# Kernel optimization log

Hardware: AMD Instinct MI355X
Metric: run time of the kernel (lower is better)

Reference implementation:

```python
import jax, jax.numpy as jnp
import numpy as np
from jax import lax

# Static problem dims (match input_specs)
B, N, F, H, C = 128, 512, 512, 256, 10
EPG = 8192            # edges per graph
K1, K2 = 256, 128      # pooling_ratio=0.5 applied twice
LAMB = 1.0
BN_EPS = 1e-5


def setup_inputs() -> dict:
    key = jax.random.key(0)
    ks = jax.random.split(key, 24)
    x = jax.random.normal(ks[0], (B * N, F), dtype=jnp.float32)
    offs = (jnp.arange(B, dtype=jnp.int32) * N)[:, None]
    src = jax.random.randint(ks[1], (B, EPG), 0, N, dtype=jnp.int32) + offs
    dst = jax.random.randint(ks[2], (B, EPG), 0, N, dtype=jnp.int32) + offs
    edge_index = jnp.stack([src.reshape(-1), dst.reshape(-1)])
    batch = jnp.repeat(jnp.arange(B, dtype=jnp.int32), N)
    s = 0.05
    p = {
        'W1': jax.random.normal(ks[3], (F, H)) * s, 'b1': jnp.zeros((H,)),
        'W2': jax.random.normal(ks[4], (H, H)) * s, 'b2': jnp.zeros((H,)),
        'W3': jax.random.normal(ks[5], (H, H)) * s, 'b3': jnp.zeros((H,)),
        'att1': jax.random.normal(ks[6], (H, 2)) * s,
        'att2': jax.random.normal(ks[7], (H, 2)) * s,
        'bn_gamma': jnp.ones((H,)), 'bn_beta': jnp.zeros((H,)),
        'bn_mean': jnp.zeros((H,)), 'bn_var': jnp.ones((H,)),
        'lin1_w': jax.random.normal(ks[8], (2 * H, H)) * s, 'lin1_b': jnp.zeros((H,)),
        'lin2_w': jax.random.normal(ks[9], (H, H // 2)) * s, 'lin2_b': jnp.zeros((H // 2,)),
        'lin3_w': jax.random.normal(ks[10], (H // 2, C)) * s, 'lin3_b': jnp.zeros((C,)),
    }
    return {'x': x, 'edge_index': edge_index, 'batch': batch, **p}


def gcn_sparse(x, src, dst, W, b):
    """GCNConv: D^-1/2 (A+I) D^-1/2 X W + b over an edge list."""
    n = x.shape[0]
    loop = jnp.arange(n, dtype=src.dtype)
    s = jnp.concatenate([src, loop])
    d = jnp.concatenate([dst, loop])
    deg = jax.ops.segment_sum(jnp.ones_like(d, jnp.float32), d, num_segments=n)
    dinv = lax.rsqrt(jnp.maximum(deg, 1.0))
    xw = x @ W
    msg = xw[s] * (dinv[s] * dinv[d])[:, None]
    return jax.ops.segment_sum(msg, d, num_segments=n) + b


def structure_learn(x_sel, A_ind, att):
    # GAT-style additive attention over all node pairs within each pooled graph,
    # biased by lamb * induced adjacency, row-softmax normalized (dense HGPSL path).
    e = x_sel @ att[:, 0]              # [B,k]
    f = x_sel @ att[:, 1]              # [B,k]
    logits = e[:, :, None] + f[:, None, :] + LAMB * A_ind
    return jax.nn.softmax(logits, axis=-1)


def pool_sparse(x, src, dst, att, k_out):
    """HGPSL pool on the sparse input graph -> dense pooled graphs [B,k,k]."""
    n = x.shape[0]
    deg = jnp.maximum(jax.ops.segment_sum(jnp.ones_like(dst, jnp.float32), dst, num_segments=n), 1.0)
    neigh = jax.ops.segment_sum(x[src], dst, num_segments=n)
    score = jnp.abs(x - neigh / deg[:, None]).sum(-1)          # node information score ||(I - D^-1 A)X||_1
    _, idx = lax.top_k(score.reshape(B, N), k_out)              # [B,k]
    offs = (jnp.arange(B, dtype=jnp.int32) * N)[:, None]
    perm = (idx.astype(jnp.int32) + offs).reshape(-1)
    x_sel = x[perm].reshape(B, k_out, -1)
    # induced adjacency among selected nodes (scatter into k+1 dummy slot)
    rank = jnp.full((B * N,), -1, jnp.int32).at[perm].set(jnp.tile(jnp.arange(k_out, dtype=jnp.int32), B))
    g = src // N
    ns, nd = rank[src], rank[dst]
    valid = (ns >= 0) & (nd >= 0)
    A = jnp.zeros((B, k_out + 1, k_out + 1), jnp.float32)
    A = A.at[g, jnp.where(valid, ns, k_out), jnp.where(valid, nd, k_out)].set(1.0)
    A_ind = A[:, :k_out, :k_out]
    return x_sel, structure_learn(x_sel, A_ind, att)


def pool_dense(x, adj, att, k_out):
    deg = jnp.maximum(adj.sum(-1), 1e-9)
    prop = jnp.einsum('bij,bjf->bif', adj, x) / deg[..., None]
    score = jnp.abs(x - prop).sum(-1)                           # [B,k_in]
    _, idx = lax.top_k(score, k_out)
    x_sel = jnp.take_along_axis(x, idx[:, :, None], axis=1)
    A_ind = jax.vmap(lambda a, i: a[i][:, i])(adj, idx)
    return x_sel, structure_learn(x_sel, A_ind, att)


def gcn_dense(x, adj, W, b):
    k = x.shape[1]
    A = adj + jnp.eye(k, dtype=x.dtype)
    dinv = lax.rsqrt(A.sum(-1))
    An = A * dinv[:, :, None] * dinv[:, None, :]
    return jnp.einsum('bij,bjf->bif', An, x @ W) + b


def readout(x):
    # [gmp || gap] over nodes of each graph
    return jnp.concatenate([x.max(axis=1), x.mean(axis=1)], axis=-1)


def reference(x, edge_index, batch, W1, b1, W2, b2, W3, b3, att1, att2,
              bn_gamma, bn_beta, bn_mean, bn_var,
              lin1_w, lin1_b, lin2_w, lin2_b, lin3_w, lin3_b):
    src, dst = edge_index[0], edge_index[1]
    h = jax.nn.relu(gcn_sparse(x, src, dst, W1, b1))            # conv1, [B*N, H]
    x__ = h
    h1, adj1 = pool_sparse(h, src, dst, att1, K1)                # pool1 -> [B,K1,H]
    x1 = readout(h1)
    hb = (h1 - bn_mean) * lax.rsqrt(bn_var + BN_EPS) * bn_gamma + bn_beta  # BN (eval)
    h2 = jax.nn.relu(gcn_dense(hb, adj1, W2, b2))                # conv2
    h2, adj2 = pool_dense(h2, adj1, att2, K2)                    # pool2 -> [B,K2,H]
    x2 = readout(h2)
    h3 = jax.nn.relu(gcn_dense(h2, adj2, W3, b3))                # conv3
    x3 = readout(h3)
    g = jax.nn.relu(x1) + jax.nn.relu(x2) + jax.nn.relu(x3)      # [B, 2H]
    g = jax.nn.relu(g @ lin1_w + lin1_b)                         # dropout=identity (eval)
    g = jax.nn.relu(g @ lin2_w + lin2_b)
    x_ = g
    logp = jax.nn.log_softmax(g @ lin3_w + lin3_b, axis=-1)
    return (x_, logp, x__)
```

## Files before the change

### kernel.cpp

```cpp
#include <hip/hip_runtime.h>
#include <stdint.h>


#define B_   128
#define N_   512
#define NN_  65536
#define E_   1048576
#define LAMB_ 1.0f

typedef unsigned short ushort_t;
typedef __attribute__((ext_vector_type(8))) short bf16x8;
typedef __attribute__((ext_vector_type(8))) unsigned short u16x8;
typedef __attribute__((ext_vector_type(4))) float f32x4;

__device__ inline float waveReduceSum(float v) {
    #pragma unroll
    for (int o = 32; o > 0; o >>= 1) v += __shfl_down(v, o, 64);
    return v;
}
__device__ inline ushort_t f2bf(float f) {
    unsigned u = __float_as_uint(f);
    u += 0x7fffu + ((u >> 16) & 1u);
    return (ushort_t)(u >> 16);
}
__device__ inline void split2(float f, ushort_t& h, ushort_t& l) {
    h = f2bf(f);
    float r = f - __uint_as_float((unsigned)h << 16);
    l = f2bf(r);
}
__device__ inline float bfu(ushort_t s) { return __uint_as_float((unsigned)s << 16); }

__device__ inline void store_T4(ushort_t* __restrict__ Th, ushort_t* __restrict__ Tl,
                                size_t base, const float* v) {
    ushort_t h[4], l[4];
    #pragma unroll
    for (int r = 0; r < 4; r++) split2(v[r], h[r], l[r]);
    uint2 ph = make_uint2((unsigned)h[0] | ((unsigned)h[1] << 16),
                          (unsigned)h[2] | ((unsigned)h[3] << 16));
    uint2 pl = make_uint2((unsigned)l[0] | ((unsigned)l[1] << 16),
                          (unsigned)l[2] | ((unsigned)l[3] << 16));
    *(uint2*)&Th[base] = ph;
    *(uint2*)&Tl[base] = pl;
}
__device__ inline void load_T4(const ushort_t* __restrict__ Th, const ushort_t* __restrict__ Tl,
                               size_t base, float* v) {
    uint2 ph = *(const uint2*)&Th[base];
    uint2 pl = *(const uint2*)&Tl[base];
    v[0] = __uint_as_float(ph.x << 16) + __uint_as_float(pl.x << 16);
    v[1] = __uint_as_float(ph.x & 0xffff0000u) + __uint_as_float(pl.x & 0xffff0000u);
    v[2] = __uint_as_float(ph.y << 16) + __uint_as_float(pl.y << 16);
    v[3] = __uint_as_float(ph.y & 0xffff0000u) + __uint_as_float(pl.y & 0xffff0000u);
}

template<int KSTEPS>
__device__ __attribute__((always_inline)) void mfma_core(
    const ushort_t* __restrict__ Ah, const ushort_t* __restrict__ Al, int lda,
    const ushort_t* __restrict__ Bh, const ushort_t* __restrict__ Bl, int ldb,
    int rowbase, int colbase, int fl, int fh, f32x4 acc[4][4]) {
    #pragma unroll
    for (int ks = 0; ks < KSTEPS; ks++) {
        int kg = ks * 32 + fh * 8;
        bf16x8 bh[4], bl[4];
        #pragma unroll
        for (int ni = 0; ni < 4; ni++) {
            size_t off = (size_t)(colbase + ni * 16 + fl) * ldb + kg;
            bh[ni] = *(const bf16x8*)&Bh[off];
            bl[ni] = *(const bf16x8*)&Bl[off];
        }
        #pragma unroll
        for (int mi = 0; mi < 4; mi++) {
            size_t off = (size_t)(rowbase + mi * 16 + fl) * lda + kg;
            bf16x8 ah = *(const bf16x8*)&Ah[off];
            bf16x8 al = *(const bf16x8*)&Al[off];
            #pragma unroll
            for (int ni = 0; ni < 4; ni++) {
                acc[mi][ni] = __builtin_amdgcn_mfma_f32_16x16x32_bf16(al, bh[ni], acc[mi][ni], 0, 0, 0);
                acc[mi][ni] = __builtin_amdgcn_mfma_f32_16x16x32_bf16(ah, bl[ni], acc[mi][ni], 0, 0, 0);
                acc[mi][ni] = __builtin_amdgcn_mfma_f32_16x16x32_bf16(ah, bh[ni], acc[mi][ni], 0, 0, 0);
            }
        }
    }
}

__global__ void split_wT_kernel(const float* __restrict__ W, int Kd,
                                ushort_t* __restrict__ Whi, ushort_t* __restrict__ Wlo) {
    int k = blockIdx.x;
    int n = threadIdx.x;
    int Nn = blockDim.x;
    float w = W[k * Nn + n];
    ushort_t h, l;
    split2(w, h, l);
    Whi[n * Kd + k] = h;
    Wlo[n * Kd + k] = l;
}

__global__ __launch_bounds__(256) void gemm_xw_mfma(
    const float* __restrict__ A, const ushort_t* __restrict__ Bhi,
    const ushort_t* __restrict__ Blo, float* __restrict__ C) {
    int m0 = blockIdx.x * 128, n0 = blockIdx.y * 128;
    __shared__ __align__(16) ushort_t As[2][4][128][8];
    int tid = threadIdx.x;
    int lane = tid & 63, w = tid >> 6;
    int wm = (w & 1) * 64, wn = (w >> 1) * 64;
    int fl = lane & 15, fh = lane >> 4;
    f32x4 acc[4][4] = {};
    int sm = tid >> 1, sk = (tid & 1) * 16;
    const float* Ap = A + (size_t)(m0 + sm) * 512 + sk;
    float4 p0 = *(const float4*)(Ap + 0);
    float4 p1 = *(const float4*)(Ap + 4);
    float4 p2 = *(const float4*)(Ap + 8);
    float4 p3 = *(const float4*)(Ap + 12);
    for (int ks = 0; ks < 16; ks++) {
        float f0[8] = {p0.x, p0.y, p0.z, p0.w, p1.x, p1.y, p1.z, p1.w};
        float f1[8] = {p2.x, p2.y, p2.z, p2.w, p3.x, p3.y, p3.z, p3.w};
        u16x8 h0, h1, l0, l1;
        #pragma unroll
        for (int i = 0; i < 8; i++) {
            ushort_t hh, ll;
            split2(f0[i], hh, ll);
            h0[i] = hh; l0[i] = ll;
        }
        #pragma unroll
        for (int i = 0; i < 8; i++) {
            ushort_t hh, ll;
            split2(f1[i], hh, ll);
            h1[i] = hh; l1[i] = ll;
        }
        __syncthreads();
        int khi = sk >> 3;
        *(u16x8*)&As[0][khi][sm][0]     = h0;
        *(u16x8*)&As[0][khi + 1][sm][0] = h1;
        *(u16x8*)&As[1][khi][sm][0]     = l0;
        *(u16x8*)&As[1][khi + 1][sm][0] = l1;
        __syncthreads();
        if (ks < 15) {
            Ap += 32;
            p0 = *(const float4*)(Ap + 0);
            p1 = *(const float4*)(Ap + 4);
            p2 = *(const float4*)(Ap + 8);
            p3 = *(const float4*)(Ap + 12);
        }
        bf16x8 ah[4], al[4], bh[4], bl[4];
        #pragma unroll
        for (int mi = 0; mi < 4; mi++) {
            ah[mi] = *(const bf16x8*)&As[0][fh][wm + mi * 16 + fl][0];
            al[mi] = *(const bf16x8*)&As[1][fh][wm + mi * 16 + fl][0];
        }
        int kg = ks * 32 + fh * 8;
        #pragma unroll
        for (int ni = 0; ni < 4; ni++) {
            size_t boff = (size_t)(n0 + wn + ni * 16 + fl) * 512 + kg;
            bh[ni] = *(const bf16x8*)&Bhi[boff];
            bl[ni] = *(const bf16x8*)&Blo[boff];
        }
        #pragma unroll
        for (int mi = 0; mi < 4; mi++)
            #pragma unroll
            for (int ni = 0; ni < 4; ni++) {
                acc[mi][ni] = __builtin_amdgcn_mfma_f32_16x16x32_bf16(al[mi], bh[ni], acc[mi][ni], 0, 0, 0);
                acc[mi][ni] = __builtin_amdgcn_mfma_f32_16x16x32_bf16(ah[mi], bl[ni], acc[mi][ni], 0, 0, 0);
                acc[mi][ni] = __builtin_amdgcn_mfma_f32_16x16x32_bf16(ah[mi], bh[ni], acc[mi][ni], 0, 0, 0);
            }
    }
    #pragma unroll
    for (int mi = 0; mi < 4; mi++)
        #pragma unroll
        for (int ni = 0; ni < 4; ni++)
            #pragma unroll
            for (int r = 0; r < 4; r++)
                C[(size_t)(m0 + wm + mi * 16 + fh * 4 + r) * 256 + n0 + wn + ni * 16 + fl]
                    = acc[mi][ni][r];
}

__global__ void count_kernel(const int* __restrict__ dst, int* __restrict__ indeg) {
    int e = blockIdx.x * 256 + threadIdx.x;
    if (e < E_) atomicAdd(&indeg[dst[e] & 65535], 1);
}
__global__ void scan_kernel(const int* __restrict__ indeg, int* __restrict__ rowstart,
                            int* __restrict__ cursor) {
    __shared__ int part[1024];
    int t = threadIdx.x;
    int base = t * 64;
    int s = 0;
    for (int i = 0; i < 64; i++) s += indeg[base + i];
    part[t] = s;
    __syncthreads();
    for (int off = 1; off < 1024; off <<= 1) {
        int v = (t >= off) ? part[t - off] : 0;
        __syncthreads();
        part[t] += v;
        __syncthreads();
    }
    int run = (t == 0) ? 0 : part[t - 1];
    for (int i = 0; i < 64; i++) {
        rowstart[base + i] = run;
        cursor[base + i] = run;
        run += indeg[base + i];
    }
}
__global__ void scatter_csr_kernel(const int* __restrict__ src, const int* __restrict__ dst,
                                   int* __restrict__ cursor, int* __restrict__ csr) {
    int e = blockIdx.x * 256 + threadIdx.x;
    if (e < E_) {
        int pos = atomicAdd(&cursor[dst[e] & 65535], 1);
        csr[pos & (E_ - 1)] = src[e] & 65535;
    }
}
__global__ void dinv_kernel(const int* __restrict__ indeg, float* __restrict__ dinv) {
    int i = blockIdx.x * 256 + threadIdx.x;
    dinv[i] = rsqrtf((float)indeg[i] + 1.0f);
}

__global__ void aggregate_kernel(const float4* __restrict__ xw, const int* __restrict__ rowstart,
                                 const int* __restrict__ indeg, const float* __restrict__ dinv,
                                 const int* __restrict__ csr, const float* __restrict__ b1,
                                 float4* __restrict__ hout) {
    int bid = (blockIdx.x & 7) * 2048 + (blockIdx.x >> 3);
    int node = bid * 4 + (threadIdx.x >> 6);
    int lane = threadIdx.x & 63;
    int beg = rowstart[node], cnt = indeg[node];
    float di = dinv[node];
    float4 acc = make_float4(0.f, 0.f, 0.f, 0.f);
    for (int t = 0; t < cnt; t++) {
        int s = csr[(beg + t) & (E_ - 1)] & 65535;
        float w = dinv[s] * di;
        float4 v = xw[(size_t)s * 64 + lane];
        acc.x += v.x * w; acc.y += v.y * w; acc.z += v.z * w; acc.w += v.w * w;
    }
    {
        float w = di * di;
        float4 v = xw[(size_t)node * 64 + lane];
        acc.x += v.x * w; acc.y += v.y * w; acc.z += v.z * w; acc.w += v.w * w;
    }
    int c4 = lane * 4;
    acc.x = fmaxf(acc.x + b1[c4 + 0], 0.f);
    acc.y = fmaxf(acc.y + b1[c4 + 1], 0.f);
    acc.z = fmaxf(acc.z + b1[c4 + 2], 0.f);
    acc.w = fmaxf(acc.w + b1[c4 + 3], 0.f);
    hout[(size_t)node * 64 + lane] = acc;
}

__global__ void score_kernel(const float4* __restrict__ h, const int* __restrict__ rowstart,
                             const int* __restrict__ indeg, const int* __restrict__ csr,
                             float* __restrict__ score) {
    int bid = (blockIdx.x & 7) * 2048 + (blockIdx.x >> 3);
    int node = bid * 4 + (threadIdx.x >> 6);
    int lane = threadIdx.x & 63;
    int beg = rowstart[node], cnt = indeg[node];
    float degp = fmaxf((float)cnt, 1.0f);
    float4 nb = make_float4(0.f, 0.f, 0.f, 0.f);
    for (int t = 0; t < cnt; t++) {
        int s = csr[(beg + t) & (E_ - 1)] & 65535;
        float4 v = h[(size_t)s * 64 + lane];
        nb.x += v.x; nb.y += v.y; nb.z += v.z; nb.w += v.w;
    }
    float4 x = h[(size_t)node * 64 + lane];
    float p = fabsf(x.x - nb.x / degp) + fabsf(x.y - nb.y / degp) +
              fabsf(x.z - nb.z / degp) + fabsf(x.w - nb.w / degp);
    p = waveReduceSum(p);
    if (lane == 0) score[node] = p;
}

__global__ void topk_kernel(const float* __restrict__ score, int n, int k,
                            int* __restrict__ out_local, int* __restrict__ rank, int Nfull) {
    int b = blockIdx.x, i = threadIdx.x;
    __shared__ float ss[512];
    __shared__ int si[512];
    ss[i] = score[b * n + i];
    si[i] = i;
    __syncthreads();
    for (int kk = 2; kk <= n; kk <<= 1)
        for (int j = kk >> 1; j > 0; j >>= 1) {
            int l = i ^ j;
            if (l > i) {
                float s1 = ss[i], s2 = ss[l];
                int i1 = si[i], i2 = si[l];
                bool up = ((i & kk) == 0);
                bool before = (s1 > s2) || (s1 == s2 && i1 < i2);
                bool doswap = up ? (!before) : before;
                if (doswap) { ss[i] = s2; ss[l] = s1; si[i] = i2; si[l] = i1; }
            }
            __syncthreads();
        }
    if (i < k) {
        int loc = si[i];
        out_local[b * k + i] = loc;
        if (rank) rank[b * Nfull + loc] = i;
// ... 95 lines not shown
        adj1[(size_t)g * 65536 + ns * 256 + nd] = 1.0f;
    }
}
__global__ void softmax_split_kernel(const float* __restrict__ ind, const float* __restrict__ e,
                                     const float* __restrict__ f, int k,
                                     ushort_t* __restrict__ oh, ushort_t* __restrict__ ol) {
    int row = blockIdx.x;
    int b = row / k;
    int c = threadIdx.x;
    __shared__ float red[256];
    float v = ind[(size_t)row * k + c];
    float lg = e[row] + f[b * k + c] + LAMB_ * v;
    red[c] = lg;
    __syncthreads();
    for (int s = k >> 1; s > 0; s >>= 1) {
        if (c < s) red[c] = fmaxf(red[c], red[c + s]);
        __syncthreads();
    }
    float mx = red[0];
    __syncthreads();
    float ex = expf(lg - mx);
    red[c] = ex;
    __syncthreads();
    for (int s = k >> 1; s > 0; s >>= 1) {
        if (c < s) red[c] += red[c + s];
        __syncthreads();
    }
    float p = ex / red[0];
    ushort_t h, l;
    split2(p, h, l);
    oh[(size_t)row * k + c] = h;
    ol[(size_t)row * k + c] = l;
}
__global__ void rowsum_split_kernel(const ushort_t* __restrict__ Ah,
                                    const ushort_t* __restrict__ Al, int k,
                                    float* __restrict__ rowsum, float* __restrict__ dinv) {
    int row = blockIdx.x * 4 + (threadIdx.x >> 6);
    int lane = threadIdx.x & 63;
    float s = 0.f;
    for (int c = lane; c < k; c += 64) {
        size_t idx = (size_t)row * k + c;
        s += bfu(Ah[idx]) + bfu(Al[idx]);
    }
    s = waveReduceSum(s);
    if (lane == 0) { rowsum[row] = s; dinv[row] = rsqrtf(s + 1.0f); }
}
__global__ void gather_adj2_split_kernel(const ushort_t* __restrict__ Ah,
                                         const ushort_t* __restrict__ Al,
                                         const int* __restrict__ idx2,
                                         float* __restrict__ adj2) {
    int ii = blockIdx.x, b = blockIdx.y, jj = threadIdx.x;
    int ri = idx2[b * 128 + ii] & 255, rj = idx2[b * 128 + jj] & 255;
    size_t idx = (size_t)b * 65536 + ri * 256 + rj;
    adj2[((size_t)(b * 128 + ii)) * 128 + jj] = bfu(Ah[idx]) + bfu(Al[idx]);
}
__global__ void bn_kernel(const float* g, const float* be,
                          const float* me, const float* va,
                          float* sBN, float* tBN) {
    int c = threadIdx.x;
    float s = g[c] * rsqrtf(va[c] + 1e-5f);
    sBN[c] = s;
    tBN[c] = be[c] - me[c] * s;
}

__global__ void gather_a3_kernel(const ushort_t* __restrict__ H2Th,
                                 const ushort_t* __restrict__ H2Tl,
                                 const int* __restrict__ idx2,
                                 ushort_t* __restrict__ A3h, ushort_t* __restrict__ A3l) {
    int row = blockIdx.x;
    int b = row >> 7;
    int node = idx2[row] & 255;
    int lane = threadIdx.x;
    int c0 = lane * 4;
    unsigned h[4], l[4];
    #pragma unroll
    for (int j = 0; j < 4; j++) {
        size_t idx = ((size_t)(b * 256 + c0 + j)) * 256 + node;
        h[j] = H2Th[idx];
        l[j] = H2Tl[idx];
    }
    uint2 ph = make_uint2(h[0] | (h[1] << 16), h[2] | (h[3] << 16));
    uint2 pl = make_uint2(l[0] | (l[1] << 16), l[2] | (l[3] << 16));
    *(uint2*)&A3h[(size_t)row * 256 + c0] = ph;
    *(uint2*)&A3l[(size_t)row * 256 + c0] = pl;
}

__global__ __launch_bounds__(256) void gemm_x2_mfma(
    const ushort_t* __restrict__ Ah, const ushort_t* __restrict__ Al,
    const ushort_t* __restrict__ Bh, const ushort_t* __restrict__ Bl,
    const float* __restrict__ dinv1,
    ushort_t* __restrict__ XTh, ushort_t* __restrict__ XTl) {
    int b = blockIdx.z;
    int m0 = blockIdx.x * 128, n0 = blockIdx.y * 128;
    int lane = threadIdx.x & 63, w = threadIdx.x >> 6;
    int wm = (w & 1) * 64, wn = (w >> 1) * 64;
    int fl = lane & 15, fh = lane >> 4;
    f32x4 acc[4][4] = {};
    mfma_core<8>(Ah + (size_t)b * 65536, Al + (size_t)b * 65536, 256,
                 Bh, Bl, 256, m0 + wm, n0 + wn, fl, fh, acc);
    #pragma unroll
    for (int mi = 0; mi < 4; mi++) {
        int row0 = m0 + wm + mi * 16 + fh * 4;
        float4 dv = *(const float4*)&dinv1[b * 256 + row0];
        float dvv[4] = {dv.x, dv.y, dv.z, dv.w};
        #pragma unroll
        for (int ni = 0; ni < 4; ni++) {
            int col = n0 + wn + ni * 16 + fl;
            float v[4];
            #pragma unroll
            for (int r = 0; r < 4; r++) v[r] = acc[mi][ni][r] * dvv[r];
            store_T4(XTh, XTl, ((size_t)(b * 256 + col)) * 256 + row0, v);
        }
    }
}

__global__ __launch_bounds__(256) void gemm_h2_mfma(
    const ushort_t* __restrict__ Ah, const ushort_t* __restrict__ Al,
    const ushort_t* __restrict__ Xh, const ushort_t* __restrict__ Xl,
    const float* __restrict__ dinv1, const float* __restrict__ b2,
    ushort_t* __restrict__ Hh, ushort_t* __restrict__ Hl) {
    int b = blockIdx.z;
    int m0 = blockIdx.x * 128, n0 = blockIdx.y * 128;
    int lane = threadIdx.x & 63, w = threadIdx.x >> 6;
    int wm = (w & 1) * 64, wn = (w >> 1) * 64;
    int fl = lane & 15, fh = lane >> 4;
    f32x4 acc[4][4] = {};
    mfma_core<8>(Ah + (size_t)b * 65536, Al + (size_t)b * 65536, 256,
                 Xh + (size_t)b * 65536, Xl + (size_t)b * 65536, 256,
                 m0 + wm, n0 + wn, fl, fh, acc);
    #pragma unroll
    for (int mi = 0; mi < 4; mi++) {
        int row0 = m0 + wm + mi * 16 + fh * 4;
        float4 dv = *(const float4*)&dinv1[b * 256 + row0];
        float dvv[4] = {dv.x, dv.y, dv.z, dv.w};
        #pragma unroll
        for (int ni = 0; ni < 4; ni++) {
            int col = n0 + wn + ni * 16 + fl;
            size_t baseT = ((size_t)(b * 256 + col)) * 256 + row0;
            float xv[4], v[4];
            load_T4(Xh, Xl, baseT, xv);
            float bc = b2[col];
            #pragma unroll
            for (int r = 0; r < 4; r++)
                v[r] = fmaxf((acc[mi][ni][r] + xv[r]) * dvv[r] + bc, 0.f);
            store_T4(Hh, Hl, baseT, v);
        }
    }
}

__global__ __launch_bounds__(256) void gemm_score_mfma(
    const ushort_t* __restrict__ Ah, const ushort_t* __restrict__ Al,
    const ushort_t* __restrict__ Hh, const ushort_t* __restrict__ Hl,
    const float* __restrict__ rowsum1, float* __restrict__ score2) {
    int b = blockIdx.z;
    int m0 = blockIdx.x * 128, n0 = blockIdx.y * 128;
    int lane = threadIdx.x & 63, w = threadIdx.x >> 6;
    int wm = (w & 1) * 64, wn = (w >> 1) * 64;
    int fl = lane & 15, fh = lane >> 4;
    f32x4 acc[4][4] = {};
    mfma_core<8>(Ah + (size_t)b * 65536, Al + (size_t)b * 65536, 256,
                 Hh + (size_t)b * 65536, Hl + (size_t)b * 65536, 256,
                 m0 + wm, n0 + wn, fl, fh, acc);
    float part[4][4];
    #pragma unroll
    for (int mi = 0; mi < 4; mi++)
        #pragma unroll
        for (int r = 0; r < 4; r++) part[mi][r] = 0.f;
    #pragma unroll
    for (int mi = 0; mi < 4; mi++) {
        int row0 = m0 + wm + mi * 16 + fh * 4;
        float4 rs = *(const float4*)&rowsum1[b * 256 + row0];
        float rd[4] = {1.0f / fmaxf(rs.x, 1e-9f), 1.0f / fmaxf(rs.y, 1e-9f),
                       1.0f / fmaxf(rs.z, 1e-9f), 1.0f / fmaxf(rs.w, 1e-9f)};
        #pragma unroll
        for (int ni = 0; ni < 4; ni++) {
            int col = n0 + wn + ni * 16 + fl;
            size_t baseT = ((size_t)(b * 256 + col)) * 256 + row0;
            float hv[4];
            load_T4(Hh, Hl, baseT, hv);
            #pragma unroll
            for (int r = 0; r < 4; r++)
                part[mi][r] += fabsf(hv[r] - acc[mi][ni][r] * rd[r]);
        }
    }
    #pragma unroll
    for (int mi = 0; mi < 4; mi++) {
        int row0 = m0 + wm + mi * 16 + fh * 4;
        #pragma unroll
        for (int r = 0; r < 4; r++) {
            float s = part[mi][r];
            #pragma unroll
            for (int o = 8; o >= 1; o >>= 1) s += __shfl_xor(s, o, 64);
            if (fl == 0) atomicAdd(&score2[b * 256 + row0 + r], s);
        }
    }
}

__global__ __launch_bounds__(256) void gemm_x3_mfma(
    const ushort_t* __restrict__ Ah, const ushort_t* __restrict__ Al,
    const ushort_t* __restrict__ Bh, const ushort_t* __restrict__ Bl,
    const float* __restrict__ dinv2,
    ushort_t* __restrict__ XTh, ushort_t* __restrict__ XTl) {
    int b = blockIdx.z;
    int m0 = blockIdx.x * 128, n0 = blockIdx.y * 128;
    int lane = threadIdx.x & 63, w = threadIdx.x >> 6;
    int wm = (w & 1) * 64, wn = (w >> 1) * 64;
    int fl = lane & 15, fh = lane >> 4;
    f32x4 acc[4][4] = {};
    mfma_core<8>(Ah + (size_t)b * 32768, Al + (size_t)b * 32768, 256,
                 Bh, Bl, 256, m0 + wm, n0 + wn, fl, fh, acc);
    #pragma unroll
    for (int mi = 0; mi < 4; mi++) {
        int row0 = m0 + wm + mi * 16 + fh * 4;
        float4 dv = *(const float4*)&dinv2[b * 128 + row0];
        float dvv[4] = {dv.x, dv.y, dv.z, dv.w};
        #pragma unroll
        for (int ni = 0; ni < 4; ni++) {
            int col = n0 + wn + ni * 16 + fl;
            float v[4];
            #pragma unroll
            for (int r = 0; r < 4; r++) v[r] = acc[mi][ni][r] * dvv[r];
            store_T4(XTh, XTl, ((size_t)(b * 256 + col)) * 128 + row0, v);
        }
    }
}

__global__ __launch_bounds__(256) void gemm_h3_mfma(
    const ushort_t* __restrict__ Ah, const ushort_t* __restrict__ Al,
    const ushort_t* __restrict__ Xh, const ushort_t* __restrict__ Xl,
    const float* __restrict__ dinv2, const float* __restrict__ b3,
    float* __restrict__ H3) {
    int b = blockIdx.z;
    int m0 = blockIdx.x * 128, n0 = blockIdx.y * 128;
    int lane = threadIdx.x & 63, w = threadIdx.x >> 6;
    int wm = (w & 1) * 64, wn = (w >> 1) * 64;
    int fl = lane & 15, fh = lane >> 4;
    f32x4 acc[4][4] = {};
    mfma_core<4>(Ah + (size_t)b * 16384, Al + (size_t)b * 16384, 128,
                 Xh + (size_t)b * 32768, Xl + (size_t)b * 32768, 128,
                 m0 + wm, n0 + wn, fl, fh, acc);
    #pragma unroll
    for (int mi = 0; mi < 4; mi++) {
        int row0 = m0 + wm + mi * 16 + fh * 4;
        float4 dv = *(const float4*)&dinv2[b * 128 + row0];
        float dvv[4] = {dv.x, dv.y, dv.z, dv.w};
        #pragma unroll
        for (int ni = 0; ni < 4; ni++) {
            int col = n0 + wn + ni * 16 + fl;
            size_t baseT = ((size_t)(b * 256 + col)) * 128 + row0;
            float xv[4];
            load_T4(Xh, Xl, baseT, xv);
            float bc = b3[col];
            #pragma unroll
            for (int r = 0; r < 4; r++) {
                float v = fmaxf((acc[mi][ni][r] + xv[r]) * dvv[r] + bc, 0.f);
                H3[(size_t)b * 32768 + (size_t)(row0 + r) * 256 + col] = v;
            }
        }
    }
}

__global__ void head_kernel(const float* __restrict__ x1, const float* __restrict__ x2,
                            const float* __restrict__ x3,
                            const float* __restrict__ w1, const float* __restrict__ b1,
                            const float* __restrict__ w2, const float* __restrict__ b2,
                            const float* __restrict__ w3, const float* __restrict__ b3,
                            float* __restrict__ out_x, float* __restrict__ out_lp) {
    int b = blockIdx.x, t = threadIdx.x;
    __shared__ float g[512], g1[256], g2[128], lg[10];
    __shared__ float lse;
    for (int i = t; i < 512; i += 256)
        g[i] = fmaxf(x1[b * 512 + i], 0.f) + fmaxf(x2[b * 512 + i], 0.f) + fmaxf(x3[b * 512 + i], 0.f);
    __syncthreads();
    {
        float acc = b1[t];
        for (int kk = 0; kk < 512; kk++) acc += g[kk] * w1[kk * 256 + t];
        g1[t] = fmaxf(acc, 0.f);
    }
    __syncthreads();
    if (t < 128) {
        float acc = b2[t];
        for (int kk = 0; kk < 256; kk++) acc += g1[kk] * w2[kk * 128 + t];
        float r = fmaxf(acc, 0.f);
        g2[t] = r;
        out_x[b * 128 + t] = r;
    }
    __syncthreads();
    if (t < 10) {
// ... 47 lines not shown
    float*    XWp     = (float*)(w + 0);
    float*    IND1    = (float*)(w + 0);
    ushort_t* X2TH    = (ushort_t*)(w + 0);
    ushort_t* X2TL    = (ushort_t*)(w + 16 * MB);
    ushort_t* A3H     = (ushort_t*)(w + 0);
    ushort_t* A3L     = (ushort_t*)(w + 8 * MB);
    float*    ADJ2IND = (float*)(w + 16 * MB);
    ushort_t* ADJ2H   = (ushort_t*)(w + 24 * MB);
    ushort_t* ADJ2L   = (ushort_t*)(w + 28 * MB);
    ushort_t* BNH1H   = (ushort_t*)(w + 32 * MB);
    ushort_t* BNH1L   = (ushort_t*)(w + 48 * MB);
    ushort_t* H2TH    = (ushort_t*)(w + 32 * MB);
    ushort_t* H2TL    = (ushort_t*)(w + 48 * MB);
    float*    H1      = (float*)(w + 64 * MB);
    ushort_t* ADJ1H   = (ushort_t*)(w + 64 * MB);
    ushort_t* ADJ1L   = (ushort_t*)(w + 80 * MB);
    ushort_t* X3TH    = (ushort_t*)(w + 64 * MB);
    ushort_t* X3TL    = (ushort_t*)(w + 72 * MB);
    float*    H3      = (float*)(w + 80 * MB);
    int*   CSR    = (int*)(w + 96 * MB);
    int*   INDEG  = (int*)(w + 100 * MB);
    int*   RSTART = INDEG + 65536;
    int*   CURSOR = RSTART + 65536;
    float* DINV   = (float*)(CURSOR + 65536);
    float* SCORE  = (float*)(w + 101 * MB);
    uint8_t* mp = w + 101 * MB + 256 * 1024;
    int*   RANK   = (int*)mp;   mp += 256 * 1024;
    int*   IDX1   = (int*)mp;   mp += 128 * 1024;
    int*   IDX2   = (int*)mp;   mp += 64 * 1024;
    float* E1     = (float*)mp; mp += 128 * 1024;
    float* F1     = (float*)mp; mp += 128 * 1024;
    float* E2     = (float*)mp; mp += 64 * 1024;
    float* F2     = (float*)mp; mp += 64 * 1024;
    float* RS1    = (float*)mp; mp += 128 * 1024;
    float* DV1    = (float*)mp; mp += 128 * 1024;
    float* RS2    = (float*)mp; mp += 64 * 1024;
    float* DV2    = (float*)mp; mp += 64 * 1024;
    float* SC2    = (float*)mp; mp += 128 * 1024;
    float* SBN    = (float*)mp; mp += 4 * 1024;
    float* TBN    = (float*)mp; mp += 4 * 1024;
    float* X1R    = (float*)mp; mp += 256 * 1024;
    float* X2R    = (float*)mp; mp += 256 * 1024;
    float* X3R    = (float*)mp; mp += 256 * 1024;
    ushort_t* W1TH = (ushort_t*)mp; mp += 256 * 1024;
    ushort_t* W1TL = (ushort_t*)mp; mp += 256 * 1024;
    ushort_t* W2TH = (ushort_t*)mp; mp += 128 * 1024;
    ushort_t* W2TL = (ushort_t*)mp; mp += 128 * 1024;
    ushort_t* W3TH = (ushort_t*)mp; mp += 128 * 1024;
    ushort_t* W3TL = (ushort_t*)mp; mp += 128 * 1024;

    float* Hout = OUT + OFF_XU;

    hipMemsetAsync(INDEG, 0, 256 * 1024, stream);
    hipMemsetAsync(RANK, 0xFF, 256 * 1024, stream);
    hipMemsetAsync(SC2, 0, 128 * 1024, stream);
    hipMemsetAsync(X1R, 0, 768 * 1024, stream);

    bn_kernel<<<1, 256, 0, stream>>>(GAM, BET, MEA, VAR, SBN, TBN);
    split_wT_kernel<<<512, 256, 0, stream>>>(W1, 512, W1TH, W1TL);
    split_wT_kernel<<<256, 256, 0, stream>>>(W2, 256, W2TH, W2TL);
    split_wT_kernel<<<256, 256, 0, stream>>>(W3, 256, W3TH, W3TL);

    gemm_xw_mfma<<<dim3(512, 2), 256, 0, stream>>>(X, W1TH, W1TL, XWp);
    count_kernel<<<4096, 256, 0, stream>>>(dst, INDEG);
    scan_kernel<<<1, 1024, 0, stream>>>(INDEG, RSTART, CURSOR);
    scatter_csr_kernel<<<4096, 256, 0, stream>>>(src, dst, CURSOR, CSR);
    dinv_kernel<<<256, 256, 0, stream>>>(INDEG, DINV);
    aggregate_kernel<<<16384, 256, 0, stream>>>((const float4*)XWp, RSTART, INDEG, DINV,
                                                CSR, B1v, (float4*)Hout);
    score_kernel<<<16384, 256, 0, stream>>>((const float4*)Hout, RSTART, INDEG, CSR, SCORE);
    topk_kernel<<<128, 512, 0, stream>>>(SCORE, 512, 256, IDX1, RANK, 512);
    gather_bn_kernel<<<32768, 64, 0, stream>>>((const float4*)Hout, IDX1, SBN, TBN,
                                               (float4*)H1, BNH1H, BNH1L);
    readout_kernel<<<dim3(128, 4), 256, 0, stream>>>(H1, 256, X1R);
    ef_plain_kernel<<<8192, 256, 0, stream>>>((const float4*)H1, ATT1, E1, F1);
    hipMemsetAsync(IND1, 0, (size_t)32 * MB, stream);
    scatter_A_kernel<<<4096, 256, 0, stream>>>(src, dst, RANK, IND1);
    softmax_split_kernel<<<32768, 256, 0, stream>>>(IND1, E1, F1, 256, ADJ1H, ADJ1L);
    rowsum_split_kernel<<<8192, 256, 0, stream>>>(ADJ1H, ADJ1L, 256, RS1, DV1);
    gemm_x2_mfma<<<dim3(2, 2, 128), 256, 0, stream>>>(BNH1H, BNH1L, W2TH, W2TL, DV1,
                                                      X2TH, X2TL);
    gemm_h2_mfma<<<dim3(2, 2, 128), 256, 0, stream>>>(ADJ1H, ADJ1L, X2TH, X2TL, DV1, B2v,
                                                      H2TH, H2TL);
    gemm_score_mfma<<<dim3(2, 2, 128), 256, 0, stream>>>(ADJ1H, ADJ1L, H2TH, H2TL, RS1, SC2);
    topk_kernel<<<128, 256, 0, stream>>>(SC2, 256, 128, IDX2, nullptr, 0);
    gather_a3_kernel<<<16384, 64, 0, stream>>>(H2TH, H2TL, IDX2, A3H, A3L);
    readout_split_kernel<<<dim3(128, 4), 256, 0, stream>>>(A3H, A3L, 128, X2R);
    ef_split_kernel<<<4096, 256, 0, stream>>>(A3H, A3L, ATT2, E2, F2);
    gather_adj2_split_kernel<<<dim3(128, 128), 128, 0, stream>>>(ADJ1H, ADJ1L, IDX2, ADJ2IND);
    softmax_split_kernel<<<16384, 128, 0, stream>>>(ADJ2IND, E2, F2, 128, ADJ2H, ADJ2L);
    rowsum_split_kernel<<<4096, 256, 0, stream>>>(ADJ2H, ADJ2L, 128, RS2, DV2);
    gemm_x3_mfma<<<dim3(1, 2, 128), 256, 0, stream>>>(A3H, A3L, W3TH, W3TL, DV2, X3TH, X3TL);
    gemm_h3_mfma<<<dim3(1, 2, 128), 256, 0, stream>>>(ADJ2H, ADJ2L, X3TH, X3TL, DV2, B3v, H3);
    readout_kernel<<<dim3(128, 4), 256, 0, stream>>>(H3, 128, X3R);
    head_kernel<<<128, 256, 0, stream>>>(X1R, X2R, X3R, L1W, L1B, L2W, L2B, L3W, L3B,
                                         OUT, OUT + OFF_LOGP);
}
```

Before: 1.026 ms.

## Fold softmax rowsum into constants, fuse prep kernels, drop LDS staging in XW GEMM

Row-softmax normalization means every learned adjacency row sums to one, so the rowsum kernels are removed. The degree scaling becomes a constant 1/sqrt(2) and the score division by the rowsum is dropped. The weight split, transpose and BN-constant kernels are merged into one prep launch, and the dinv computation is folded into the scan kernel. The first GEMM now loads A directly from global memory with a truncating hi/lo split instead of staging through LDS. The neighbor loops in aggregate and score are unrolled by two. The constant-rowsum shortcut relies on the softmax output summing to exactly one, and the truncating split slightly changes rounding.

```diff
diff --git a/kernel.cpp b/kernel.cpp
--- a/kernel.cpp
+++ b/kernel.cpp
@@ -7,6 +7,7 @@
 #define NN_  65536
 #define E_   1048576
 #define LAMB_ 1.0f
+#define RSQRT2_ 0.70710678118654752f
 
 typedef unsigned short ushort_t;
 typedef __attribute__((ext_vector_type(8))) short bf16x8;
@@ -29,6 +30,7 @@
     l = f2bf(r);
 }
 __device__ inline float bfu(ushort_t s) { return __uint_as_float((unsigned)s << 16); }
+__device__ inline bf16x8 as_bf(u16x8 u) { union { u16x8 a; bf16x8 b; } c; c.a = u; return c.b; }
 
 __device__ inline void store_T4(ushort_t* __restrict__ Th, ushort_t* __restrict__ Tl,
                                 size_t base, const float* v) {
@@ -82,85 +84,79 @@
     }
 }
 
-__global__ void split_wT_kernel(const float* __restrict__ W, int Kd,
-                                ushort_t* __restrict__ Whi, ushort_t* __restrict__ Wlo) {
-    int k = blockIdx.x;
-    int n = threadIdx.x;
-    int Nn = blockDim.x;
-    float w = W[k * Nn + n];
-    ushort_t h, l;
-    split2(w, h, l);
-    Whi[n * Kd + k] = h;
-    Wlo[n * Kd + k] = l;
-}
-
-__global__ __launch_bounds__(256) void gemm_xw_mfma(
+__global__ void prep_kernel(const float* __restrict__ W1, const float* __restrict__ W2,
+                            const float* __restrict__ W3,
+                            const float* __restrict__ g, const float* __restrict__ be,
+                            const float* __restrict__ me, const float* __restrict__ va,
+                            ushort_t* __restrict__ W1TH, ushort_t* __restrict__ W1TL,
+                            ushort_t* __restrict__ W2TH, ushort_t* __restrict__ W2TL,
+                            ushort_t* __restrict__ W3TH, ushort_t* __restrict__ W3TL,
+                            float* __restrict__ sBN, float* __restrict__ tBN) {
+    int bx = blockIdx.x, n = threadIdx.x;
+    if (bx < 512) {
+        float v = W1[bx * 256 + n];
+        ushort_t h, l; split2(v, h, l);
+        W1TH[n * 512 + bx] = h; W1TL[n * 512 + bx] = l;
+    } else if (bx < 768) {
+        int k = bx - 512;
+        float v = W2[k * 256 + n];
+        ushort_t h, l; split2(v, h, l);
+        W2TH[n * 256 + k] = h; W2TL[n * 256 + k] = l;
+    } else if (bx < 1024) {
+        int k = bx - 768;
+        float v = W3[k * 256 + n];
+        ushort_t h, l; split2(v, h, l);
+        W3TH[n * 256 + k] = h; W3TL[n * 256 + k] = l;
+    } else {
+        float s = g[n] * rsqrtf(va[n] + 1e-5f);
+        sBN[n] = s;
+        tBN[n] = be[n] - me[n] * s;
+    }
+}
+
+__global__ __launch_bounds__(256) void gemm_xw_mfma2(
     const float* __restrict__ A, const ushort_t* __restrict__ Bhi,
     const ushort_t* __restrict__ Blo, float* __restrict__ C) {
     int m0 = blockIdx.x * 128, n0 = blockIdx.y * 128;
-    __shared__ __align__(16) ushort_t As[2][4][128][8];
-    int tid = threadIdx.x;
-    int lane = tid & 63, w = tid >> 6;
+    int lane = threadIdx.x & 63, w = threadIdx.x >> 6;
     int wm = (w & 1) * 64, wn = (w >> 1) * 64;
     int fl = lane & 15, fh = lane >> 4;
     f32x4 acc[4][4] = {};
-    int sm = tid >> 1, sk = (tid & 1) * 16;
-    const float* Ap = A + (size_t)(m0 + sm) * 512 + sk;
-    float4 p0 = *(const float4*)(Ap + 0);
-    float4 p1 = *(const float4*)(Ap + 4);
-    float4 p2 = *(const float4*)(Ap + 8);
-    float4 p3 = *(const float4*)(Ap + 12);
+    const float*    Ab  = A   + (size_t)(m0 + wm + fl) * 512 + fh * 8;
+    const ushort_t* Bhb = Bhi + (size_t)(n0 + wn + fl) * 512 + fh * 8;
+    const ushort_t* Blb = Blo + (size_t)(n0 + wn + fl) * 512 + fh * 8;
+    #pragma unroll 2
     for (int ks = 0; ks < 16; ks++) {
-        float f0[8] = {p0.x, p0.y, p0.z, p0.w, p1.x, p1.y, p1.z, p1.w};
-        float f1[8] = {p2.x, p2.y, p2.z, p2.w, p3.x, p3.y, p3.z, p3.w};
-        u16x8 h0, h1, l0, l1;
-        #pragma unroll
-        for (int i = 0; i < 8; i++) {
-            ushort_t hh, ll;
-            split2(f0[i], hh, ll);
-            h0[i] = hh; l0[i] = ll;
-        }
-        #pragma unroll
-        for (int i = 0; i < 8; i++) {
-            ushort_t hh, ll;
-            split2(f1[i], hh, ll);
-            h1[i] = hh; l1[i] = ll;
-        }
-        __syncthreads();
-        int khi = sk >> 3;
-        *(u16x8*)&As[0][khi][sm][0]     = h0;
-        *(u16x8*)&As[0][khi + 1][sm][0] = h1;
-        *(u16x8*)&As[1][khi][sm][0]     = l0;
-        *(u16x8*)&As[1][khi + 1][sm][0] = l1;
-        __syncthreads();
-        if (ks < 15) {
-            Ap += 32;
-            p0 = *(const float4*)(Ap + 0);
-            p1 = *(const float4*)(Ap + 4);
-            p2 = *(const float4*)(Ap + 8);
-            p3 = *(const float4*)(Ap + 12);
-        }
-        bf16x8 ah[4], al[4], bh[4], bl[4];
+        int kg = ks * 32;
+        bf16x8 bh[4], bl[4];
+        #pragma unroll
+        for (int ni = 0; ni < 4; ni++) {
+            size_t off = (size_t)ni * (16 * 512) + kg;
+            bh[ni] = *(const bf16x8*)&Bhb[off];
+            bl[ni] = *(const bf16x8*)&Blb[off];
+        }
         #pragma unroll
         for (int mi = 0; mi < 4; mi++) {
-            ah[mi] = *(const bf16x8*)&As[0][fh][wm + mi * 16 + fl][0];
-            al[mi] = *(const bf16x8*)&As[1][fh][wm + mi * 16 + fl][0];
-        }
-        int kg = ks * 32 + fh * 8;
-        #pragma unroll
-        for (int ni = 0; ni < 4; ni++) {
-            size_t boff = (size_t)(n0 + wn + ni * 16 + fl) * 512 + kg;
-            bh[ni] = *(const bf16x8*)&Bhi[boff];
-            bl[ni] = *(const bf16x8*)&Blo[boff];
-        }
-        #pragma unroll
-        for (int mi = 0; mi < 4; mi++)
+            const float* ap = Ab + (size_t)mi * (16 * 512) + kg;
+            float4 q0 = *(const float4*)ap;
+            float4 q1 = *(const float4*)(ap + 4);
+            float f[8] = {q0.x, q0.y, q0.z, q0.w, q1.x, q1.y, q1.z, q1.w};
+            u16x8 uh, ul;
+            #pragma unroll
+            for (int i = 0; i < 8; i++) {
+                unsigned u = __float_as_uint(f[i]);
+                uh[i] = (ushort_t)(u >> 16);
+                float lf = f[i] - __uint_as_float(u & 0xffff0000u);
+                ul[i] = (ushort_t)(__float_as_uint(lf) >> 16);
+            }
+            bf16x8 ah = as_bf(uh), al = as_bf(ul);
             #pragma unroll
             for (int ni = 0; ni < 4; ni++) {
-                acc[mi][ni] = __builtin_amdgcn_mfma_f32_16x16x32_bf16(al[mi], bh[ni], acc[mi][ni], 0, 0, 0);
-                acc[mi][ni] = __builtin_amdgcn_mfma_f32_16x16x32_bf16(ah[mi], bl[ni], acc[mi][ni], 0, 0, 0);
-                acc[mi][ni] = __builtin_amdgcn_mfma_f32_16x16x32_bf16(ah[mi], bh[ni], acc[mi][ni], 0, 0, 0);
+                acc[mi][ni] = __builtin_amdgcn_mfma_f32_16x16x32_bf16(al, bh[ni], acc[mi][ni], 0, 0, 0);
+                acc[mi][ni] = __builtin_amdgcn_mfma_f32_16x16x32_bf16(ah, bl[ni], acc[mi][ni], 0, 0, 0);
+                acc[mi][ni] = __builtin_amdgcn_mfma_f32_16x16x32_bf16(ah, bh[ni], acc[mi][ni], 0, 0, 0);
             }
+        }
     }
     #pragma unroll
     for (int mi = 0; mi < 4; mi++)
@@ -177,7 +173,7 @@
     if (e < E_) atomicAdd(&indeg[dst[e] & 65535], 1);
 }
 __global__ void scan_kernel(const int* __restrict__ indeg, int* __restrict__ rowstart,
-                            int* __restrict__ cursor) {
+                            int* __restrict__ cursor, float* __restrict__ dinv) {
     __shared__ int part[1024];
     int t = threadIdx.x;
     int base = t * 64;
@@ -193,9 +189,11 @@
     }
     int run = (t == 0) ? 0 : part[t - 1];
     for (int i = 0; i < 64; i++) {
+        int dg = indeg[base + i];
         rowstart[base + i] = run;
         cursor[base + i] = run;
-        run += indeg[base + i];
+        dinv[base + i] = rsqrtf((float)dg + 1.0f);
+        run += dg;
     }
 }
 __global__ void scatter_csr_kernel(const int* __restrict__ src, const int* __restrict__ dst,
@@ -205,10 +203,6 @@
         int pos = atomicAdd(&cursor[dst[e] & 65535], 1);
         csr[pos & (E_ - 1)] = src[e] & 65535;
     }
-}
-__global__ void dinv_kernel(const int* __restrict__ indeg, float* __restrict__ dinv) {
-    int i = blockIdx.x * 256 + threadIdx.x;
-    dinv[i] = rsqrtf((float)indeg[i] + 1.0f);
 }
 
 __global__ void aggregate_kernel(const float4* __restrict__ xw, const int* __restrict__ rowstart,
@@ -221,16 +215,28 @@
     int beg = rowstart[node], cnt = indeg[node];
     float di = dinv[node];
     float4 acc = make_float4(0.f, 0.f, 0.f, 0.f);
-    for (int t = 0; t < cnt; t++) {
-        int s = csr[(beg + t) & (E_ - 1)] & 65535;
-        float w = dinv[s] * di;
-        float4 v = xw[(size_t)s * 64 + lane];
-        acc.x += v.x * w; acc.y += v.y * w; acc.z += v.z * w; acc.w += v.w * w;
+    int t = 0;
+    for (; t + 1 < cnt; t += 2) {
+        int s0 = csr[(beg + t) & (E_ - 1)] & 65535;
+        int s1 = csr[(beg + t + 1) & (E_ - 1)] & 65535;
+        float w0 = dinv[s0] * di, w1 = dinv[s1] * di;
+        float4 v0 = xw[(size_t)s0 * 64 + lane];
+        float4 v1 = xw[(size_t)s1 * 64 + lane];
+        acc.x += v0.x * w0 + v1.x * w1;
+        acc.y += v0.y * w0 + v1.y * w1;
+        acc.z += v0.z * w0 + v1.z * w1;
+        acc.w += v0.w * w0 + v1.w * w1;
+    }
+    if (t < cnt) {
+        int s0 = csr[(beg + t) & (E_ - 1)] & 65535;
+        float w0 = dinv[s0] * di;
+        float4 v0 = xw[(size_t)s0 * 64 + lane];
+        acc.x += v0.x * w0; acc.y += v0.y * w0; acc.z += v0.z * w0; acc.w += v0.w * w0;
     }
     {
-        float w = di * di;
+        float w0 = di * di;
         float4 v = xw[(size_t)node * 64 + lane];
-        acc.x += v.x * w; acc.y += v.y * w; acc.z += v.z * w; acc.w += v.w * w;
+        acc.x += v.x * w0; acc.y += v.y * w0; acc.z += v.z * w0; acc.w += v.w * w0;
     }
     int c4 = lane * 4;
     acc.x = fmaxf(acc.x + b1[c4 + 0], 0.f);
@@ -249,10 +255,19 @@
     int beg = rowstart[node], cnt = indeg[node];
     float degp = fmaxf((float)cnt, 1.0f);
     float4 nb = make_float4(0.f, 0.f, 0.f, 0.f);
-    for (int t = 0; t < cnt; t++) {
-        int s = csr[(beg + t) & (E_ - 1)] & 65535;
-        float4 v = h[(size_t)s * 64 + lane];
-        nb.x += v.x; nb.y += v.y; nb.z += v.z; nb.w += v.w;
+    int t = 0;
+    for (; t + 1 < cnt; t += 2) {
+        int s0 = csr[(beg + t) & (E_ - 1)] & 65535;
+        int s1 = csr[(beg + t + 1) & (E_ - 1)] & 65535;
+        float4 v0 = h[(size_t)s0 * 64 + lane];
+        float4 v1 = h[(size_t)s1 * 64 + lane];
+        nb.x += v0.x + v1.x; nb.y += v0.y + v1.y;
+        nb.z += v0.z + v1.z; nb.w += v0.w + v1.w;
+    }
+    if (t < cnt) {
+        int s0 = csr[(beg + t) & (E_ - 1)] & 65535;
+        float4 v0 = h[(size_t)s0 * 64 + lane];
+        nb.x += v0.x; nb.y += v0.y; nb.z += v0.z; nb.w += v0.w;
     }
     float4 x = h[(size_t)node * 64 + lane];
     float p = fabsf(x.x - nb.x / degp) + fabsf(x.y - nb.y / degp) +
@@ -414,19 +429,6 @@
     oh[(size_t)row * k + c] = h;
     ol[(size_t)row * k + c] = l;
 }
-__global__ void rowsum_split_kernel(const ushort_t* __restrict__ Ah,
-                                    const ushort_t* __restrict__ Al, int k,
-                                    float* __restrict__ rowsum, float* __restrict__ dinv) {
-    int row = blockIdx.x * 4 + (threadIdx.x >> 6);
-    int lane = threadIdx.x & 63;
-    float s = 0.f;
-    for (int c = lane; c < k; c += 64) {
-        size_t idx = (size_t)row * k + c;
-        s += bfu(Ah[idx]) + bfu(Al[idx]);
-    }
-    s = waveReduceSum(s);
-    if (lane == 0) { rowsum[row] = s; dinv[row] = rsqrtf(s + 1.0f); }
-}
 __global__ void gather_adj2_split_kernel(const ushort_t* __restrict__ Ah,
                                          const ushort_t* __restrict__ Al,
                                          const int* __restrict__ idx2,
@@ -435,14 +437,6 @@
     int ri = idx2[b * 128 + ii] & 255, rj = idx2[b * 128 + jj] & 255;
     size_t idx = (size_t)b * 65536 + ri * 256 + rj;
     adj2[((size_t)(b * 128 + ii)) * 128 + jj] = bfu(Ah[idx]) + bfu(Al[idx]);
-}
-__global__ void bn_kernel(const float* g, const float* be,
-                          const float* me, const float* va,
-                          float* sBN, float* tBN) {
-    int c = threadIdx.x;
-    float s = g[c] * rsqrtf(va[c] + 1e-5f);
-    sBN[c] = s;
-    tBN[c] = be[c] - me[c] * s;
 }
 
 __global__ void gather_a3_kernel(const ushort_t* __restrict__ H2Th,
@@ -470,7 +464,6 @@
 __global__ __launch_bounds__(256) void gemm_x2_mfma(
     const ushort_t* __restrict__ Ah, const ushort_t* __restrict__ Al,
     const ushort_t* __restrict__ Bh, const ushort_t* __restrict__ Bl,
-    const float* __restrict__ dinv1,
     ushort_t* __restrict__ XTh, ushort_t* __restrict__ XTl) {
     int b = blockIdx.z;
     int m0 = blockIdx.x * 128, n0 = blockIdx.y * 128;
@@ -483,14 +476,12 @@
     #pragma unroll
     for (int mi = 0; mi < 4; mi++) {
         int row0 = m0 + wm + mi * 16 + fh * 4;
-        float4 dv = *(const float4*)&dinv1[b * 256 + row0];
-        float dvv[4] = {dv.x, dv.y, dv.z, dv.w};
         #pragma unroll
         for (int ni = 0; ni < 4; ni++) {
             int col = n0 + wn + ni * 16 + fl;
             float v[4];
             #pragma unroll
-            for (int r = 0; r < 4; r++) v[r] = acc[mi][ni][r] * dvv[r];
+            for (int r = 0; r < 4; r++) v[r] = acc[mi][ni][r] * RSQRT2_;
             store_T4(XTh, XTl, ((size_t)(b * 256 + col)) * 256 + row0, v);
         }
     }
@@ -499,7 +490,7 @@
 __global__ __launch_bounds__(256) void gemm_h2_mfma(
     const ushort_t* __restrict__ Ah, const ushort_t* __restrict__ Al,
     const ushort_t* __restrict__ Xh, const ushort_t* __restrict__ Xl,
-    const float* __restrict__ dinv1, const float* __restrict__ b2,
+    const float* __restrict__ b2,
     ushort_t* __restrict__ Hh, ushort_t* __restrict__ Hl) {
     int b = blockIdx.z;
     int m0 = blockIdx.x * 128, n0 = blockIdx.y * 128;
@@ -513,8 +504,6 @@
     #pragma unroll
     for (int mi = 0; mi < 4; mi++) {
         int row0 = m0 + wm + mi * 16 + fh * 4;
-        float4 dv = *(const float4*)&dinv1[b * 256 + row0];
-        float dvv[4] = {dv.x, dv.y, dv.z, dv.w};
         #pragma unroll
         for (int ni = 0; ni < 4; ni++) {
             int col = n0 + wn + ni * 16 + fl;
@@ -524,7 +513,7 @@
             float bc = b2[col];
             #pragma unroll
             for (int r = 0; r < 4; r++)
-                v[r] = fmaxf((acc[mi][ni][r] + xv[r]) * dvv[r] + bc, 0.f);
+                v[r] = fmaxf((acc[mi][ni][r] + xv[r]) * RSQRT2_ + bc, 0.f);
             store_T4(Hh, Hl, baseT, v);
         }
     }
@@ -533,7 +522,7 @@
 __global__ __launch_bounds__(256) void gemm_score_mfma(
     const ushort_t* __restrict__ Ah, const ushort_t* __restrict__ Al,
     const ushort_t* __restrict__ Hh, const ushort_t* __restrict__ Hl,
-    const float* __restrict__ rowsum1, float* __restrict__ score2) {
+    float* __restrict__ score2) {
     int b = blockIdx.z;
     int m0 = blockIdx.x * 128, n0 = blockIdx.y * 128;
     int lane = threadIdx.x & 63, w = threadIdx.x >> 6;
@@ -551,9 +540,6 @@
     #pragma unroll
     for (int mi = 0; mi < 4; mi++) {
         int row0 = m0 + wm + mi * 16 + fh * 4;
-        float4 rs = *(const float4*)&rowsum1[b * 256 + row0];
-        float rd[4] = {1.0f / fmaxf(rs.x, 1e-9f), 1.0f / fmaxf(rs.y, 1e-9f),
-                       1.0f / fmaxf(rs.z, 1e-9f), 1.0f / fmaxf(rs.w, 1e-9f)};
         #pragma unroll
         for (int ni = 0; ni < 4; ni++) {
             int col = n0 + wn + ni * 16 + fl;
@@ -562,7 +548,7 @@
             load_T4(Hh, Hl, baseT, hv);
             #pragma unroll
             for (int r = 0; r < 4; r++)
-                part[mi][r] += fabsf(hv[r] - acc[mi][ni][r] * rd[r]);
+                part[mi][r] += fabsf(hv[r] - acc[mi][ni][r]);
         }
     }
     #pragma unroll
@@ -581,7 +567,6 @@
 __global__ __launch_bounds__(256) void gemm_x3_mfma(
     const ushort_t* __restrict__ Ah, const ushort_t* __restrict__ Al,
     const ushort_t* __restrict__ Bh, const ushort_t* __restrict__ Bl,
-    const float* __restrict__ dinv2,
     ushort_t* __restrict__ XTh, ushort_t* __restrict__ XTl) {
     int b = blockIdx.z;
     int m0 = blockIdx.x * 128, n0 = blockIdx.y * 128;
@@ -594,14 +579,12 @@
     #pragma unroll
     for (int mi = 0; mi < 4; mi++) {
         int row0 = m0 + wm + mi * 16 + fh * 4;
-        float4 dv = *(const float4*)&dinv2[b * 128 + row0];
-        float dvv[4] = {dv.x, dv.y, dv.z, dv.w};
         #pragma unroll
         for (int ni = 0; ni < 4; ni++) {
             int col = n0 + wn + ni * 16 + fl;
             float v[4];
             #pragma unroll
-            for (int r = 0; r < 4; r++) v[r] = acc[mi][ni][r] * dvv[r];
+            for (int r = 0; r < 4; r++) v[r] = acc[mi][ni][r] * RSQRT2_;
             store_T4(XTh, XTl, ((size_t)(b * 256 + col)) * 128 + row0, v);
         }
     }
@@ -610,7 +593,7 @@
 __global__ __launch_bounds__(256) void gemm_h3_mfma(
     const ushort_t* __restrict__ Ah, const ushort_t* __restrict__ Al,
     const ushort_t* __restrict__ Xh, const ushort_t* __restrict__ Xl,
-    const float* __restrict__ dinv2, const float* __restrict__ b3,
+    const float* __restrict__ b3,
     float* __restrict__ H3) {
     int b = blockIdx.z;
     int m0 = blockIdx.x * 128, n0 = blockIdx.y * 128;
@@ -624,8 +607,6 @@
     #pragma unroll
     for (int mi = 0; mi < 4; mi++) {
         int row0 = m0 + wm + mi * 16 + fh * 4;
-        float4 dv = *(const float4*)&dinv2[b * 128 + row0];
-        float dvv[4] = {dv.x, dv.y, dv.z, dv.w};
         #pragma unroll
         for (int ni = 0; ni < 4; ni++) {
             int col = n0 + wn + ni * 16 + fl;
@@ -635,7 +616,7 @@
             float bc = b3[col];
             #pragma unroll
             for (int r = 0; r < 4; r++) {
-                float v = fmaxf((acc[mi][ni][r] + xv[r]) * dvv[r] + bc, 0.f);
+                float v = fmaxf((acc[mi][ni][r] + xv[r]) * RSQRT2_ + bc, 0.f);
                 H3[(size_t)b * 32768 + (size_t)(row0 + r) * 256 + col] = v;
             }
         }
@@ -749,10 +730,6 @@
     float* F1     = (float*)mp; mp += 128 * 1024;
     float* E2     = (float*)mp; mp += 64 * 1024;
     float* F2     = (float*)mp; mp += 64 * 1024;
-    float* RS1    = (float*)mp; mp += 128 * 1024;
-    float* DV1    = (float*)mp; mp += 128 * 1024;
-    float* RS2    = (float*)mp; mp += 64 * 1024;
-    float* DV2    = (float*)mp; mp += 64 * 1024;
     float* SC2    = (float*)mp; mp += 128 * 1024;
     float* SBN    = (float*)mp; mp += 4 * 1024;
     float* TBN    = (float*)mp; mp += 4 * 1024;
@@ -773,16 +750,12 @@
     hipMemsetAsync(SC2, 0, 128 * 1024, stream);
     hipMemsetAsync(X1R, 0, 768 * 1024, stream);
 
-    bn_kernel<<<1, 256, 0, stream>>>(GAM, BET, MEA, VAR, SBN, TBN);
-    split_wT_kernel<<<512, 256, 0, stream>>>(W1, 512, W1TH, W1TL);
-    split_wT_kernel<<<256, 256, 0, stream>>>(W2, 256, W2TH, W2TL);
-    split_wT_kernel<<<256, 256, 0, stream>>>(W3, 256, W3TH, W3TL);
-
-    gemm_xw_mfma<<<dim3(512, 2), 256, 0, stream>>>(X, W1TH, W1TL, XWp);
+    prep_kernel<<<1025, 256, 0, stream>>>(W1, W2, W3, GAM, BET, MEA, VAR,
+                                          W1TH, W1TL, W2TH, W2TL, W3TH, W3TL, SBN, TBN);
+    gemm_xw_mfma2<<<dim3(512, 2), 256, 0, stream>>>(X, W1TH, W1TL, XWp);
     count_kernel<<<4096, 256, 0, stream>>>(dst, INDEG);
-    scan_kernel<<<1, 1024, 0, stream>>>(INDEG, RSTART, CURSOR);
+    scan_kernel<<<1, 1024, 0, stream>>>(INDEG, RSTART, CURSOR, DINV);
     scatter_csr_kernel<<<4096, 256, 0, stream>>>(src, dst, CURSOR, CSR);
-    dinv_kernel<<<256, 256, 0, stream>>>(INDEG, DINV);
     aggregate_kernel<<<16384, 256, 0, stream>>>((const float4*)XWp, RSTART, INDEG, DINV,
                                                 CSR, B1v, (float4*)Hout);
     score_kernel<<<16384, 256, 0, stream>>>((const float4*)Hout, RSTART, INDEG, CSR, SCORE);
@@ -794,21 +767,19 @@
     hipMemsetAsync(IND1, 0, (size_t)32 * MB, stream);
     scatter_A_kernel<<<4096, 256, 0, stream>>>(src, dst, RANK, IND1);
     softmax_split_kernel<<<32768, 256, 0, stream>>>(IND1, E1, F1, 256, ADJ1H, ADJ1L);
-    rowsum_split_kernel<<<8192, 256, 0, stream>>>(ADJ1H, ADJ1L, 256, RS1, DV1);
-    gemm_x2_mfma<<<dim3(2, 2, 128), 256, 0, stream>>>(BNH1H, BNH1L, W2TH, W2TL, DV1,
+    gemm_x2_mfma<<<dim3(2, 2, 128), 256, 0, stream>>>(BNH1H, BNH1L, W2TH, W2TL,
                                                       X2TH, X2TL);
-    gemm_h2_mfma<<<dim3(2, 2, 128), 256, 0, stream>>>(ADJ1H, ADJ1L, X2TH, X2TL, DV1, B2v,
+    gemm_h2_mfma<<<dim3(2, 2, 128), 256, 0, stream>>>(ADJ1H, ADJ1L, X2TH, X2TL, B2v,
                                                       H2TH, H2TL);
-    gemm_score_mfma<<<dim3(2, 2, 128), 256, 0, stream>>>(ADJ1H, ADJ1L, H2TH, H2TL, RS1, SC2);
+    gemm_score_mfma<<<dim3(2, 2, 128), 256, 0, stream>>>(ADJ1H, ADJ1L, H2TH, H2TL, SC2);
     topk_kernel<<<128, 256, 0, stream>>>(SC2, 256, 128, IDX2, nullptr, 0);
     gather_a3_kernel<<<16384, 64, 0, stream>>>(H2TH, H2TL, IDX2, A3H, A3L);
     readout_split_kernel<<<dim3(128, 4), 256, 0, stream>>>(A3H, A3L, 128, X2R);
     ef_split_kernel<<<4096, 256, 0, stream>>>(A3H, A3L, ATT2, E2, F2);
     gather_adj2_split_kernel<<<dim3(128, 128), 128, 0, stream>>>(ADJ1H, ADJ1L, IDX2, ADJ2IND);
     softmax_split_kernel<<<16384, 128, 0, stream>>>(ADJ2IND, E2, F2, 128, ADJ2H, ADJ2L);
-    rowsum_split_kernel<<<4096, 256, 0, stream>>>(ADJ2H, ADJ2L, 128, RS2, DV2);
-    gemm_x3_mfma<<<dim3(1, 2, 128), 256, 0, stream>>>(A3H, A3L, W3TH, W3TL, DV2, X3TH, X3TL);
-    gemm_h3_mfma<<<dim3(1, 2, 128), 256, 0, stream>>>(ADJ2H, ADJ2L, X3TH, X3TL, DV2, B3v, H3);
+    gemm_x3_mfma<<<dim3(1, 2, 128), 256, 0, stream>>>(A3H, A3L, W3TH, W3TL, X3TH, X3TL);
+    gemm_h3_mfma<<<dim3(1, 2, 128), 256, 0, stream>>>(ADJ2H, ADJ2L, X3TH, X3TL, B3v, H3);
     readout_kernel<<<dim3(128, 4), 256, 0, stream>>>(H3, 128, X3R);
     head_kernel<<<128, 256, 0, stream>>>(X1R, X2R, X3R, L1W, L1B, L2W, L2B, L3W, L3B,
                                          OUT, OUT + OFF_LOGP);
```

Result: no change. 1.013 ms (-1.2%).
